# Performance work log

Hardware: AMD Instinct MI355X
Metric: run time of the kernel (lower is better)

Reference implementation:

```python
import jax, jax.numpy as jnp
import numpy as np

B, C, N, K, C_OUT = 4, 64, 8192, 16, 64


def setup_inputs() -> dict:
    key = jax.random.key(0)
    k1, k2, k3, k4 = jax.random.split(key, 4)
    x = jax.random.normal(k1, (B, C, N, 1), dtype=jnp.float32)
    edge_index = jax.random.randint(k2, (2, B, N, K), 0, N, dtype=jnp.int64)
    # 1x1 conv weights of BasicConv([2C, C_OUT]) -> [C_OUT, 2C]
    W = jax.random.normal(k3, (C_OUT, 2 * C), dtype=jnp.float32) * (1.0 / np.sqrt(2 * C))
    b = jax.random.normal(k4, (C_OUT,), dtype=jnp.float32) * 0.01
    return {"x": x, "edge_index": edge_index, "W": W, "b": b}


def _batched_index_select(x, idx):
    # x: [B, C, N] ; idx: [B, N, K] -> [B, C, N, K]
    b, c, n = x.shape
    k = idx.shape[-1]
    flat = jnp.broadcast_to(idx.reshape(b, 1, n * k), (b, c, n * k))
    return jnp.take_along_axis(x, flat, axis=2).reshape(b, c, n, k)


def reference(x, edge_index, W, b):
    xs = x[..., 0]                                  # [B, C, N]
    x_i = _batched_index_select(xs, edge_index[1])  # [B, C, N, K] central nodes
    x_j = _batched_index_select(xs, edge_index[0])  # [B, C, N, K] neighbors
    feat = jnp.concatenate([x_i, x_j - x_i], axis=1)  # [B, 2C, N, K]
    # 1x1 conv: [C_OUT, 2C] x [B, 2C, N, K] -> [B, C_OUT, N, K], + bias, ReLU (norm=None)
    h = jnp.einsum('oc,bcnk->bonk', W, feat) + b[None, :, None, None]
    h = jax.nn.relu(h)
    # max over neighbors, keepdim on last axis -> [B, C_OUT, N, 1]
    return jnp.max(h, axis=-1, keepdims=True)
```

## Files before the change

### kernel.cpp

```cpp
#include <hip/hip_runtime.h>


#define BB   4
#define CCH  64
#define NN   8192
#define KK   16

typedef _Float16 h2 __attribute__((ext_vector_type(2)));
typedef _Float16 h4 __attribute__((ext_vector_type(4)));

__global__ __launch_bounds__(256) void gemm_kernel(const float* __restrict__ x,
                                                   const float* __restrict__ W,
                                                   _Float16* __restrict__ y) {
    __shared__ float wT[64 * 132];
    __shared__ float xs[64 * 64];

    const int t   = threadIdx.x;
    const int blk = blockIdx.x;
    const int xcd  = blk & 7;
    const int b    = xcd >> 1;
    const int tile = ((blk >> 3) << 1) | (xcd & 1);
    const int n0   = tile * 64;

    {
        const int sbase = t >> 6;
        const int k     = t & 63;
        #pragma unroll
        for (int i = 0; i < 32; ++i) {
            const int s = sbase + (i << 2);
            float v;
            if (s < CCH) v = W[s * 128 + k] - W[s * 128 + 64 + k];
            else         v = W[(s - CCH) * 128 + 64 + k];
            wT[k * 132 + s] = v;
        }
    }
    {
        const float* xb = x + (size_t)b * CCH * NN + n0;
        #pragma unroll
        for (int i = 0; i < 16; ++i) {
            const int e = t + (i << 8);
            const int k = e >> 6, n = e & 63;
            xs[k * 64 + n] = xb[(size_t)k * NN + n];
        }
    }
    __syncthreads();

    const int c_grp = t & 31;
    const int n_grp = t >> 5;

    float acc[4][8];
    #pragma unroll
    for (int i = 0; i < 4; ++i)
        #pragma unroll
        for (int j = 0; j < 8; ++j) acc[i][j] = 0.f;

    #pragma unroll 8
    for (int k = 0; k < 64; ++k) {
        const float4 wv  = *(const float4*)&wT[k * 132 + 4 * c_grp];
        const float4 xv0 = *(const float4*)&xs[k * 64 + 8 * n_grp];
        const float4 xv1 = *(const float4*)&xs[k * 64 + 8 * n_grp + 4];
        const float wa[4] = {wv.x, wv.y, wv.z, wv.w};
        const float xa[8] = {xv0.x, xv0.y, xv0.z, xv0.w, xv1.x, xv1.y, xv1.z, xv1.w};
        #pragma unroll
        for (int i = 0; i < 4; ++i)
            #pragma unroll
            for (int j = 0; j < 8; ++j)
                acc[i][j] += wa[i] * xa[j];
    }

    _Float16* ybp = y + ((size_t)b * NN + n0) * 128 + 4 * c_grp;
    #pragma unroll
    for (int j = 0; j < 8; ++j) {
        h4 v;
        v.x = (_Float16)acc[0][j]; v.y = (_Float16)acc[1][j];
        v.z = (_Float16)acc[2][j]; v.w = (_Float16)acc[3][j];
        *(h4*)&ybp[(size_t)(8 * n_grp + j) * 128] = v;
    }
}

__global__ __launch_bounds__(256) void gather_kernel(const _Float16* __restrict__ y,
                                                     const int* __restrict__ edge,
                                                     const float* __restrict__ bias,
                                                     float* __restrict__ out) {
    __shared__ int   eL[16][2][16];
    __shared__ float so[16][65];

    const int t   = threadIdx.x;
    const int blk = blockIdx.x;
    const int xcd  = blk & 7;
    const int b    = xcd >> 1;
    const int tile = ((blk >> 3) << 1) | (xcd & 1);
    const int n0   = tile * 16;

    if (t < 128) {
        const int src = t >> 6;
        const int f   = (t & 63) << 2;
        const int nl  = f >> 4, k0 = f & 15;
        const size_t eb = (size_t)(src == 0 ? BB + b : b) * NN * KK;
        *(int4*)&eL[nl][src][k0] = *(const int4*)&edge[eb + (size_t)(n0 + nl) * KK + k0];
    }
    __syncthreads();

    const int w    = t >> 6;
    const int lane = t & 63;
    const int half = lane >> 5;
    const int cl   = lane & 31;

    const float2 bv = *(const float2*)&bias[2 * cl];
    const _Float16* yb = y + (size_t)b * NN * 128;

    #pragma unroll 2
    for (int u = 0; u < 4; ++u) {
        const int nl = 4 * w + u;
        h2 s[8];
        #pragma unroll
        for (int kp = 0; kp < 8; ++kp) {
            const int k  = 2 * kp + half;
            const int i1 = eL[nl][0][k];
            const int i0 = eL[nl][1][k];
            const uint a = *(const uint*)&yb[(size_t)i1 * 128 + 2 * cl];
            const uint c = *(const uint*)&yb[(size_t)i0 * 128 + 64 + 2 * cl];
            union { uint u32; h2 h; } ua, uc;
            ua.u32 = a; uc.u32 = c;
            s[kp] = ua.h + uc.h;
        }
        h2 m = s[0];
        #pragma unroll
        for (int kp = 1; kp < 8; ++kp) m = __builtin_elementwise_max(m, s[kp]);
        union { int i32; h2 h; } um, uo;
        um.h = m;
        uo.i32 = __shfl_xor(um.i32, 32, 64);
        m = __builtin_elementwise_max(m, uo.h);
        if (half == 0) {
            float2 r;
            r.x = fmaxf((float)m.x + bv.x, 0.f);
            r.y = fmaxf((float)m.y + bv.y, 0.f);
            *(float2*)&so[nl][2 * cl] = r;
        }
    }
    __syncthreads();

    {
        const int c = t >> 2;
        const int q = t & 3;
        float4 v;
        v.x = so[4 * q + 0][c];
        v.y = so[4 * q + 1][c];
        v.z = so[4 * q + 2][c];
        v.w = so[4 * q + 3][c];
        *(float4*)(out + ((size_t)b * CCH + c) * NN + n0 + 4 * q) = v;
    }
}

extern "C" void kernel_launch(void* const* d_in, const int* in_sizes, int n_in,
                              void* d_out, int out_size, void* d_ws, size_t ws_size,
                              hipStream_t stream) {
    (void)in_sizes; (void)n_in; (void)out_size; (void)ws_size;
    const float* x    = (const float*)d_in[0];
    const int*   edge = (const int*)d_in[1];
    const float* W    = (const float*)d_in[2];
    const float* bias = (const float*)d_in[3];
    float*       out  = (float*)d_out;
    _Float16*    y    = (_Float16*)d_ws;

    gemm_kernel<<<dim3(512), dim3(256), 0, stream>>>(x, W, y);
    gather_kernel<<<dim3(2048), dim3(256), 0, stream>>>(y, edge, bias, out);
}
```

Baseline: 27.99 us.

## Assign gather tiles by hardware XCC id via atomic counters; nontemporal edge/out

The gather kernel now reads the hardware XCC id and takes a tile slot from a per-XCC atomic counter, so each XCD processes exactly the batch whose y slice it shares in L2. The grid is doubled, and surplus blocks exit immediately. The gemm kernel resets the counters. Edge loads and output stores become nontemporal to avoid polluting cache. This adds an atomic plus a block sync per workgroup and over-launches blocks. Correctness relies on each XCC getting at least 256 blocks.

```diff
diff --git a/kernel.cpp b/kernel.cpp
--- a/kernel.cpp
+++ b/kernel.cpp
@@ -5,18 +5,24 @@
 #define CCH  64
 #define NN   8192
 #define KK   16
+#define CNT_STRIDE 32
 
 typedef _Float16 h2 __attribute__((ext_vector_type(2)));
 typedef _Float16 h4 __attribute__((ext_vector_type(4)));
+typedef int      v4i __attribute__((ext_vector_type(4)));
+typedef float    v4f __attribute__((ext_vector_type(4)));
 
 __global__ __launch_bounds__(256) void gemm_kernel(const float* __restrict__ x,
                                                    const float* __restrict__ W,
-                                                   _Float16* __restrict__ y) {
+                                                   _Float16* __restrict__ y,
+                                                   int* __restrict__ cnt) {
     __shared__ float wT[64 * 132];
     __shared__ float xs[64 * 64];
 
     const int t   = threadIdx.x;
     const int blk = blockIdx.x;
+    if (blk == 0 && t < 8) cnt[t * CNT_STRIDE] = 0;
+
     const int xcd  = blk & 7;
     const int b    = xcd >> 1;
     const int tile = ((blk >> 3) << 1) | (xcd & 1);
@@ -81,23 +87,34 @@
 __global__ __launch_bounds__(256) void gather_kernel(const _Float16* __restrict__ y,
                                                      const int* __restrict__ edge,
                                                      const float* __restrict__ bias,
-                                                     float* __restrict__ out) {
+                                                     float* __restrict__ out,
+                                                     int* __restrict__ cnt) {
+    __shared__ int   s_tile;
     __shared__ int   eL[16][2][16];
     __shared__ float so[16][65];
 
-    const int t   = threadIdx.x;
-    const int blk = blockIdx.x;
-    const int xcd  = blk & 7;
-    const int b    = xcd >> 1;
-    const int tile = ((blk >> 3) << 1) | (xcd & 1);
-    const int n0   = tile * 16;
+    const int t = threadIdx.x;
+    if (t == 0) {
+        unsigned xcc;
+        asm volatile("s_getreg_b32 %0, hwreg(HW_REG_XCC_ID)" : "=s"(xcc));
+        const int x    = (int)(xcc & 7u);
+        const int slot = atomicAdd(&cnt[x * CNT_STRIDE], 1);
+        s_tile = (slot < 256) ? (x * 256 + slot) : -1;
+    }
+    __syncthreads();
+    const int tile = s_tile;
+    if (tile < 0) return;
+
+    const int b  = tile >> 9;
+    const int n0 = (tile & 511) * 16;
 
     if (t < 128) {
         const int src = t >> 6;
         const int f   = (t & 63) << 2;
         const int nl  = f >> 4, k0 = f & 15;
         const size_t eb = (size_t)(src == 0 ? BB + b : b) * NN * KK;
-        *(int4*)&eL[nl][src][k0] = *(const int4*)&edge[eb + (size_t)(n0 + nl) * KK + k0];
+        *(v4i*)&eL[nl][src][k0] =
+            __builtin_nontemporal_load((const v4i*)&edge[eb + (size_t)(n0 + nl) * KK + k0]);
     }
     __syncthreads();
 
@@ -143,12 +160,12 @@
     {
         const int c = t >> 2;
         const int q = t & 3;
-        float4 v;
+        v4f v;
         v.x = so[4 * q + 0][c];
         v.y = so[4 * q + 1][c];
         v.z = so[4 * q + 2][c];
         v.w = so[4 * q + 3][c];
-        *(float4*)(out + ((size_t)b * CCH + c) * NN + n0 + 4 * q) = v;
+        __builtin_nontemporal_store(v, (v4f*)(out + ((size_t)b * CCH + c) * NN + n0 + 4 * q));
     }
 }
 
@@ -162,7 +179,8 @@
     const float* bias = (const float*)d_in[3];
     float*       out  = (float*)d_out;
     _Float16*    y    = (_Float16*)d_ws;
+    int*         cnt  = (int*)((char*)d_ws + (8u << 20));
 
-    gemm_kernel<<<dim3(512), dim3(256), 0, stream>>>(x, W, y);
-    gather_kernel<<<dim3(2048), dim3(256), 0, stream>>>(y, edge, bias, out);
+    gemm_kernel<<<dim3(512), dim3(256), 0, stream>>>(x, W, y, cnt);
+    gather_kernel<<<dim3(4096), dim3(256), 0, stream>>>(y, edge, bias, out, cnt);
 }
```

New measurement: 32.69 us. 16.8% more time.

## Stage channel-group slices of projected features in LDS for gather

Applied to the files above, without the earlier changes.

The GEMM output is rewritten into a channel-group-major layout, split into two buffers of 4 channels across all nodes. Each gather block then loads one 4-channel slice for its whole batch into 128 KB of shared memory and does the random neighbor lookups from LDS instead of global memory. Each thread handles one node, reads all 16 edge indices as vectors and writes outputs directly. The costs are 16x redundant edge-index reads across channel groups, a single-block-per-CU occupancy limit, and a heavy LDS fill per block.

```diff
diff --git a/kernel.cpp b/kernel.cpp
--- a/kernel.cpp
+++ b/kernel.cpp
@@ -6,14 +6,15 @@
 #define NN   8192
 #define KK   16
 
-typedef _Float16 h2 __attribute__((ext_vector_type(2)));
 typedef _Float16 h4 __attribute__((ext_vector_type(4)));
+typedef int      v4i __attribute__((ext_vector_type(4)));
 
 __global__ __launch_bounds__(256) void gemm_kernel(const float* __restrict__ x,
                                                    const float* __restrict__ W,
-                                                   _Float16* __restrict__ y) {
-    __shared__ float wT[64 * 132];
-    __shared__ float xs[64 * 64];
+                                                   _Float16* __restrict__ y1g,
+                                                   _Float16* __restrict__ y2g) {
+    __shared__ __align__(16) float wT[64 * 132];
+    __shared__ __align__(16) float xs[64 * 64];
 
     const int t   = threadIdx.x;
     const int blk = blockIdx.x;
@@ -68,88 +69,100 @@
                 acc[i][j] += wa[i] * xa[j];
     }
 
-    _Float16* ybp = y + ((size_t)b * NN + n0) * 128 + 4 * c_grp;
+    __syncthreads();
+    _Float16* sy16 = (_Float16*)wT;
     #pragma unroll
     for (int j = 0; j < 8; ++j) {
+        const int n = 8 * n_grp + j;
         h4 v;
         v.x = (_Float16)acc[0][j]; v.y = (_Float16)acc[1][j];
         v.z = (_Float16)acc[2][j]; v.w = (_Float16)acc[3][j];
-        *(h4*)&ybp[(size_t)(8 * n_grp + j) * 128] = v;
+        *(h4*)&sy16[n * 132 + 4 * c_grp] = v;
+    }
+    __syncthreads();
+    {
+        const int g  = t >> 4;
+        const int nl = t & 15;
+        #pragma unroll
+        for (int it = 0; it < 4; ++it) {
+            const int n = nl + 16 * it;
+            const h4 a1 = *(const h4*)&sy16[n * 132 + 4 * g];
+            const h4 a2 = *(const h4*)&sy16[n * 132 + 64 + 4 * g];
+            const size_t off = ((size_t)(b * 16 + g) * NN + n0 + n) * 4;
+            *(h4*)&y1g[off] = a1;
+            *(h4*)&y2g[off] = a2;
+        }
     }
 }
 
-__global__ __launch_bounds__(256) void gather_kernel(const _Float16* __restrict__ y,
-                                                     const int* __restrict__ edge,
-                                                     const float* __restrict__ bias,
-                                                     float* __restrict__ out) {
-    __shared__ int   eL[16][2][16];
-    __shared__ float so[16][65];
+__global__ __launch_bounds__(256, 1) void gather_kernel(const _Float16* __restrict__ y1g,
+                                                        const _Float16* __restrict__ y2g,
+                                                        const int* __restrict__ edge,
+                                                        const float* __restrict__ bias,
+                                                        float* __restrict__ out) {
+    __shared__ __align__(16) _Float16 sy1[NN * 4];
+    __shared__ __align__(16) _Float16 sy2[NN * 4];
 
-    const int t   = threadIdx.x;
-    const int blk = blockIdx.x;
-    const int xcd  = blk & 7;
-    const int b    = xcd >> 1;
-    const int tile = ((blk >> 3) << 1) | (xcd & 1);
-    const int n0   = tile * 16;
+    const int t     = threadIdx.x;
+    const int blk   = blockIdx.x;
+    const int b     = blk >> 6;
+    const int g     = (blk >> 2) & 15;
+    const int chunk = blk & 3;
 
-    if (t < 128) {
-        const int src = t >> 6;
-        const int f   = (t & 63) << 2;
-        const int nl  = f >> 4, k0 = f & 15;
-        const size_t eb = (size_t)(src == 0 ? BB + b : b) * NN * KK;
-        *(int4*)&eL[nl][src][k0] = *(const int4*)&edge[eb + (size_t)(n0 + nl) * KK + k0];
-    }
-    __syncthreads();
-
-    const int w    = t >> 6;
-    const int lane = t & 63;
-    const int half = lane >> 5;
-    const int cl   = lane & 31;
-
-    const float2 bv = *(const float2*)&bias[2 * cl];
-    const _Float16* yb = y + (size_t)b * NN * 128;
-
-    #pragma unroll 2
-    for (int u = 0; u < 4; ++u) {
-        const int nl = 4 * w + u;
-        h2 s[8];
+    {
+        const _Float16* y1s = y1g + (size_t)(b * 16 + g) * NN * 4;
+        const _Float16* y2s = y2g + (size_t)(b * 16 + g) * NN * 4;
         #pragma unroll
-        for (int kp = 0; kp < 8; ++kp) {
-            const int k  = 2 * kp + half;
-            const int i1 = eL[nl][0][k];
-            const int i0 = eL[nl][1][k];
-            const uint a = *(const uint*)&yb[(size_t)i1 * 128 + 2 * cl];
-            const uint c = *(const uint*)&yb[(size_t)i0 * 128 + 64 + 2 * cl];
-            union { uint u32; h2 h; } ua, uc;
-            ua.u32 = a; uc.u32 = c;
-            s[kp] = ua.h + uc.h;
-        }
-        h2 m = s[0];
-        #pragma unroll
-        for (int kp = 1; kp < 8; ++kp) m = __builtin_elementwise_max(m, s[kp]);
-        union { int i32; h2 h; } um, uo;
-        um.h = m;
-        uo.i32 = __shfl_xor(um.i32, 32, 64);
-        m = __builtin_elementwise_max(m, uo.h);
-        if (half == 0) {
-            float2 r;
-            r.x = fmaxf((float)m.x + bv.x, 0.f);
-            r.y = fmaxf((float)m.y + bv.y, 0.f);
-            *(float2*)&so[nl][2 * cl] = r;
+        for (int i = 0; i < 16; ++i) {
+            const int e = (i * 256 + t) * 8;
+            *(v4i*)&sy1[e] = *(const v4i*)&y1s[e];
+            *(v4i*)&sy2[e] = *(const v4i*)&y2s[e];
         }
     }
     __syncthreads();
 
-    {
-        const int c = t >> 2;
-        const int q = t & 3;
-        float4 v;
-        v.x = so[4 * q + 0][c];
-        v.y = so[4 * q + 1][c];
-        v.z = so[4 * q + 2][c];
-        v.w = so[4 * q + 3][c];
-        *(float4*)(out + ((size_t)b * CCH + c) * NN + n0 + 4 * q) = v;
+    const float4 bv = *(const float4*)&bias[4 * g];
+    const int* e1p = edge + (size_t)(BB + b) * NN * KK;
+    const int* e0p = edge + (size_t)b * NN * KK;
+    const int cbase = chunk * 2048;
+
+#define EDGE_TERM(I1, I0) ({                                   \
+        const h4 a_ = *(const h4*)&sy1[(size_t)(unsigned)(I1) * 4]; \
+        const h4 c_ = *(const h4*)&sy2[(size_t)(unsigned)(I0) * 4]; \
+        a_ + c_; })
+
+    #pragma unroll 2
+    for (int it = 0; it < 8; ++it) {
+        const int n = cbase + it * 256 + t;
+        const v4i* p1 = (const v4i*)&e1p[(size_t)n * KK];
+        const v4i* p0 = (const v4i*)&e0p[(size_t)n * KK];
+        const v4i A1 = p1[0], B1 = p1[1], C1 = p1[2], D1 = p1[3];
+        const v4i A0 = p0[0], B0 = p0[1], C0 = p0[2], D0 = p0[3];
+
+        h4 m = EDGE_TERM(A1.x, A0.x);
+        m = __builtin_elementwise_max(m, EDGE_TERM(A1.y, A0.y));
+        m = __builtin_elementwise_max(m, EDGE_TERM(A1.z, A0.z));
+        m = __builtin_elementwise_max(m, EDGE_TERM(A1.w, A0.w));
+        m = __builtin_elementwise_max(m, EDGE_TERM(B1.x, B0.x));
+        m = __builtin_elementwise_max(m, EDGE_TERM(B1.y, B0.y));
+        m = __builtin_elementwise_max(m, EDGE_TERM(B1.z, B0.z));
+        m = __builtin_elementwise_max(m, EDGE_TERM(B1.w, B0.w));
+        m = __builtin_elementwise_max(m, EDGE_TERM(C1.x, C0.x));
+        m = __builtin_elementwise_max(m, EDGE_TERM(C1.y, C0.y));
+        m = __builtin_elementwise_max(m, EDGE_TERM(C1.z, C0.z));
+        m = __builtin_elementwise_max(m, EDGE_TERM(C1.w, C0.w));
+        m = __builtin_elementwise_max(m, EDGE_TERM(D1.x, D0.x));
+        m = __builtin_elementwise_max(m, EDGE_TERM(D1.y, D0.y));
+        m = __builtin_elementwise_max(m, EDGE_TERM(D1.z, D0.z));
+        m = __builtin_elementwise_max(m, EDGE_TERM(D1.w, D0.w));
+
+        float* ob = out + ((size_t)b * CCH + 4 * g) * NN + n;
+        ob[0]          = fmaxf((float)m.x + bv.x, 0.f);
+        ob[NN]         = fmaxf((float)m.y + bv.y, 0.f);
+        ob[2 * (size_t)NN] = fmaxf((float)m.z + bv.z, 0.f);
+        ob[3 * (size_t)NN] = fmaxf((float)m.w + bv.w, 0.f);
     }
+#undef EDGE_TERM
 }
 
 extern "C" void kernel_launch(void* const* d_in, const int* in_sizes, int n_in,
@@ -161,8 +174,9 @@
     const float* W    = (const float*)d_in[2];
     const float* bias = (const float*)d_in[3];
     float*       out  = (float*)d_out;
-    _Float16*    y    = (_Float16*)d_ws;
+    _Float16*    y1g  = (_Float16*)d_ws;
+    _Float16*    y2g  = (_Float16*)((char*)d_ws + (4u << 20));
 
-    gemm_kernel<<<dim3(512), dim3(256), 0, stream>>>(x, W, y);
-    gather_kernel<<<dim3(2048), dim3(256), 0, stream>>>(y, edge, bias, out);
+    gemm_kernel<<<dim3(512), dim3(256), 0, stream>>>(x, W, y1g, y2g);
+    gather_kernel<<<dim3(256), dim3(256), 0, stream>>>(y1g, y2g, edge, bias, out);
 }
```

Measured after the change: 31.59 us. +12.9%, slower.

## Restructure gather kernel to one node per lane with 16-byte vector loads

Applied to the files above, without the earlier changes.

The gather kernel now gives each lane one node and each wave an 8-channel slice. Each lane loops over all 16 neighbours with 16-byte half8 loads and keeps a running max in registers, which removes the cross-half shuffle and the short 4-byte loads. Blocks grow to 512 threads covering 64 nodes, and the XCD-aware block mapping is dropped. The trade-off is that neighbouring lanes now read scattered rows rather than contiguous channels, so coalescing within a wave may suffer, and there are fewer blocks in the grid.

```diff
diff --git a/kernel.cpp b/kernel.cpp
--- a/kernel.cpp
+++ b/kernel.cpp
@@ -6,8 +6,10 @@
 #define NN   8192
 #define KK   16
 
-typedef _Float16 h2 __attribute__((ext_vector_type(2)));
 typedef _Float16 h4 __attribute__((ext_vector_type(4)));
+typedef _Float16 h8 __attribute__((ext_vector_type(8)));
+typedef int      v4i __attribute__((ext_vector_type(4)));
+typedef float    v4f __attribute__((ext_vector_type(4)));
 
 __global__ __launch_bounds__(256) void gemm_kernel(const float* __restrict__ x,
                                                    const float* __restrict__ W,
@@ -78,77 +80,72 @@
     }
 }
 
-__global__ __launch_bounds__(256) void gather_kernel(const _Float16* __restrict__ y,
+__global__ __launch_bounds__(512) void gather_kernel(const _Float16* __restrict__ y,
                                                      const int* __restrict__ edge,
                                                      const float* __restrict__ bias,
                                                      float* __restrict__ out) {
-    __shared__ int   eL[16][2][16];
-    __shared__ float so[16][65];
+    __shared__ int   eL[64][2][17];
+    __shared__ float sm[64][66];
 
     const int t   = threadIdx.x;
     const int blk = blockIdx.x;
-    const int xcd  = blk & 7;
-    const int b    = xcd >> 1;
-    const int tile = ((blk >> 3) << 1) | (xcd & 1);
-    const int n0   = tile * 16;
+    const int b   = blk >> 7;
+    const int n0  = (blk & 127) * 64;
 
-    if (t < 128) {
-        const int src = t >> 6;
-        const int f   = (t & 63) << 2;
-        const int nl  = f >> 4, k0 = f & 15;
-        const size_t eb = (size_t)(src == 0 ? BB + b : b) * NN * KK;
-        *(int4*)&eL[nl][src][k0] = *(const int4*)&edge[eb + (size_t)(n0 + nl) * KK + k0];
+    {
+        const int src = t >> 8;
+        const int n   = (t >> 2) & 63;
+        const int kq  = (t & 3) * 4;
+        const size_t ebase = (size_t)(src == 0 ? BB + b : b) * NN * KK;
+        *(v4i*)&eL[n][src][kq] = *(const v4i*)&edge[ebase + (size_t)(n0 + n) * KK + kq];
     }
     __syncthreads();
 
     const int w    = t >> 6;
     const int lane = t & 63;
-    const int half = lane >> 5;
-    const int cl   = lane & 31;
-
-    const float2 bv = *(const float2*)&bias[2 * cl];
+    const int co   = w * 8;
     const _Float16* yb = y + (size_t)b * NN * 128;
 
-    #pragma unroll 2
-    for (int u = 0; u < 4; ++u) {
-        const int nl = 4 * w + u;
-        h2 s[8];
+    h8 m;
+    #pragma unroll 4
+    for (int k = 0; k < 16; ++k) {
+        const int i1 = eL[lane][0][k];
+        const int i0 = eL[lane][1][k];
+        const h8 a = *(const h8*)&yb[(size_t)i1 * 128 + co];
+        const h8 c = *(const h8*)&yb[(size_t)i0 * 128 + 64 + co];
+        const h8 s = a + c;
+        m = (k == 0) ? s : __builtin_elementwise_max(m, s);
+    }
+
+    {
+        const v4f b0 = *(const v4f*)&bias[co];
+        const v4f b1 = *(const v4f*)&bias[co + 4];
+        float r[8];
+        r[0] = fmaxf((float)m[0] + b0.x, 0.f);
+        r[1] = fmaxf((float)m[1] + b0.y, 0.f);
+        r[2] = fmaxf((float)m[2] + b0.z, 0.f);
+        r[3] = fmaxf((float)m[3] + b0.w, 0.f);
+        r[4] = fmaxf((float)m[4] + b1.x, 0.f);
+        r[5] = fmaxf((float)m[5] + b1.y, 0.f);
+        r[6] = fmaxf((float)m[6] + b1.z, 0.f);
+        r[7] = fmaxf((float)m[7] + b1.w, 0.f);
         #pragma unroll
-        for (int kp = 0; kp < 8; ++kp) {
-            const int k  = 2 * kp + half;
-            const int i1 = eL[nl][0][k];
-            const int i0 = eL[nl][1][k];
-            const uint a = *(const uint*)&yb[(size_t)i1 * 128 + 2 * cl];
-            const uint c = *(const uint*)&yb[(size_t)i0 * 128 + 64 + 2 * cl];
-            union { uint u32; h2 h; } ua, uc;
-            ua.u32 = a; uc.u32 = c;
-            s[kp] = ua.h + uc.h;
-        }
-        h2 m = s[0];
-        #pragma unroll
-        for (int kp = 1; kp < 8; ++kp) m = __builtin_elementwise_max(m, s[kp]);
-        union { int i32; h2 h; } um, uo;
-        um.h = m;
-        uo.i32 = __shfl_xor(um.i32, 32, 64);
-        m = __builtin_elementwise_max(m, uo.h);
-        if (half == 0) {
-            float2 r;
-            r.x = fmaxf((float)m.x + bv.x, 0.f);
-            r.y = fmaxf((float)m.y + bv.y, 0.f);
-            *(float2*)&so[nl][2 * cl] = r;
-        }
+        for (int j = 0; j < 4; ++j)
+            *(float2*)&sm[lane][co + 2 * j] = make_float2(r[2 * j], r[2 * j + 1]);
     }
     __syncthreads();
 
-    {
-        const int c = t >> 2;
-        const int q = t & 3;
-        float4 v;
-        v.x = so[4 * q + 0][c];
-        v.y = so[4 * q + 1][c];
-        v.z = so[4 * q + 2][c];
-        v.w = so[4 * q + 3][c];
-        *(float4*)(out + ((size_t)b * CCH + c) * NN + n0 + 4 * q) = v;
+    #pragma unroll
+    for (int r2 = 0; r2 < 2; ++r2) {
+        const int idx = t + (r2 << 9);
+        const int c   = idx >> 4;
+        const int q   = idx & 15;
+        v4f v;
+        v.x = sm[4 * q + 0][c];
+        v.y = sm[4 * q + 1][c];
+        v.z = sm[4 * q + 2][c];
+        v.w = sm[4 * q + 3][c];
+        *(v4f*)(out + ((size_t)b * CCH + c) * NN + n0 + 4 * q) = v;
     }
 }
 
@@ -164,5 +161,5 @@
     _Float16*    y    = (_Float16*)d_ws;
 
     gemm_kernel<<<dim3(512), dim3(256), 0, stream>>>(x, W, y);
-    gather_kernel<<<dim3(2048), dim3(256), 0, stream>>>(y, edge, bias, out);
+    gather_kernel<<<dim3(512), dim3(512), 0, stream>>>(y, edge, bias, out);
 }
```

After: 56.21 us. 101% more time.
